# Kernel optimization log

Hardware: AMD Instinct MI355X
Metric: run time of the kernel (lower is better)

The kernel has to match this reference:

```python
import jax, jax.numpy as jnp
import numpy as np

NUM_EXPERTS = 8
TOP_K = 2
HIDDEN = 1024
INTER = 2048
BATCH, SEQ = 2, 2048


def setup_inputs() -> dict:
    key = jax.random.key(0)
    k1, k2, k3, k4 = jax.random.split(key, 4)
    hidden_states = jax.random.normal(k1, (BATCH, SEQ, HIDDEN), dtype=jnp.float32)
    # 0.02 init scale keeps router softmax unsaturated and activations sane
    router_w = jax.random.normal(k2, (NUM_EXPERTS, HIDDEN), dtype=jnp.float32) * 0.02
    up_w = jax.random.normal(k3, (NUM_EXPERTS, HIDDEN, INTER), dtype=jnp.float32) * 0.02
    down_w = jax.random.normal(k4, (NUM_EXPERTS, INTER, HIDDEN), dtype=jnp.float32) * 0.02
    return {"hidden_states": hidden_states, "router_w": router_w, "up_w": up_w, "down_w": down_w}


def reference(hidden_states, router_w, up_w, down_w):
    batch, seq_len, hidden = hidden_states.shape
    flat = hidden_states.reshape(-1, hidden)            # [N, H]
    num_tokens = flat.shape[0]

    router_logits = flat @ router_w.T                   # [N, E]
    router_probs = jax.nn.softmax(router_logits, axis=-1)
    top_weights, top_indices = jax.lax.top_k(router_probs, TOP_K)  # [N, k]
    top_weights = top_weights / jnp.sum(top_weights, axis=-1, keepdims=True)

    # scatter normalized top-k weights into a dense [N, E] mask
    rows = jnp.arange(num_tokens)[:, None]
    expert_mask = jnp.zeros((num_tokens, NUM_EXPERTS), dtype=flat.dtype)
    expert_mask = expert_mask.at[rows, top_indices].set(top_weights)

    # dense path: all experts on all tokens via batched matmul
    h = jnp.einsum('nh,ehf->enf', flat, up_w)           # [E, N, F]
    h = jax.nn.gelu(h, approximate=False)               # torch nn.GELU default = erf
    expert_out = jnp.einsum('enf,efh->enh', h, down_w)  # [E, N, H]
    output = jnp.einsum('enh,ne->nh', expert_out, expert_mask)
    output = output.reshape(batch, seq_len, hidden)

    # load-balancing aux loss; f is computed under no_grad in torch
    one_hot = jnp.zeros((num_tokens, NUM_EXPERTS), dtype=jnp.float32)
    one_hot = one_hot.at[rows, top_indices].set(1.0)
    f = jax.lax.stop_gradient(jnp.sum(one_hot, axis=0) / (num_tokens * TOP_K))
    P = jnp.mean(router_probs, axis=0)
    aux_loss = NUM_EXPERTS * jnp.sum(f * P)
    return output, aux_loss
```

## Files before the change

### kernel.cpp

```cpp
#include <hip/hip_runtime.h>
#include <math.h>

#define NE 8
#define HD 1024
#define FD 2048
#define NT 4096
#define NSLOT (NT * 2)

typedef __attribute__((ext_vector_type(8))) _Float16 half8;
typedef __attribute__((ext_vector_type(4))) float floatx4;

__device__ __forceinline__ void gload_lds(const _Float16* g, _Float16* l) {
  __builtin_amdgcn_global_load_lds(
      (const __attribute__((address_space(1))) unsigned int*)g,
      (__attribute__((address_space(3))) unsigned int*)l, 16, 0, 0);
}

__global__ __launch_bounds__(256) void transpose_cvt(const float* __restrict__ in,
                                                     _Float16* __restrict__ outp,
                                                     int R, int C) {
  __shared__ float t[32][132];
  int e = blockIdx.z;
  int r0 = blockIdx.x * 32, c0 = blockIdx.y * 128;
  int tid = threadIdx.x;
  int f4c = tid & 31, rr = tid >> 5;
  const float* src = in + (size_t)e * R * C;
#pragma unroll
  for (int i = 0; i < 4; i++) {
    float4 v = *(const float4*)(src + (size_t)(r0 + rr + 8 * i) * C + c0 + f4c * 4);
    *(float4*)&t[rr + 8 * i][f4c * 4] = v;
  }
  __syncthreads();
  _Float16* dst = outp + (size_t)e * R * C;
  int oc = tid >> 1, rh = (tid & 1) * 16;
  union { _Float16 h[8]; uint4 v; } o;
#pragma unroll
  for (int k2 = 0; k2 < 2; k2++) {
#pragma unroll
    for (int k = 0; k < 8; k++) o.h[k] = (_Float16)t[rh + k2 * 8 + k][oc];
    *(uint4*)(dst + (size_t)(c0 + oc) * R + r0 + rh + k2 * 8) = o.v;
  }
}

__global__ __launch_bounds__(256) void router_probs_kernel(
    const float* __restrict__ x, const float* __restrict__ rw, _Float16* __restrict__ xh,
    float* __restrict__ probs, int* __restrict__ sel_e, float* __restrict__ sel_w) {
  int n = blockIdx.x * 4 + (threadIdx.x >> 6);
  int lane = threadIdx.x & 63;
  const float* xr = x + (size_t)n * HD;
  float xv[16];
#pragma unroll
  for (int t = 0; t < 16; t++) xv[t] = xr[lane + 64 * t];
  _Float16* xhr = xh + (size_t)n * HD;
#pragma unroll
  for (int t = 0; t < 16; t++) xhr[lane + 64 * t] = (_Float16)xv[t];
  float logits[NE];
#pragma unroll
  for (int e = 0; e < NE; e++) {
    const float* w = rw + (size_t)e * HD;
    float acc = 0.f;
#pragma unroll
    for (int t = 0; t < 16; t++) acc += xv[t] * w[lane + 64 * t];
    for (int off = 32; off > 0; off >>= 1) acc += __shfl_down(acc, off);
    logits[e] = acc;
  }
  if (lane == 0) {
    float mx = logits[0];
#pragma unroll
    for (int e = 1; e < NE; e++) mx = fmaxf(mx, logits[e]);
    float p[NE]; float s = 0.f;
#pragma unroll
    for (int e = 0; e < NE; e++) { p[e] = expf(logits[e] - mx); s += p[e]; }
    float inv = 1.f / s;
#pragma unroll
    for (int e = 0; e < NE; e++) { p[e] *= inv; probs[n * NE + e] = p[e]; }
    int i1 = 0;
#pragma unroll
    for (int e = 1; e < NE; e++) if (p[e] > p[i1]) i1 = e;
    int i2 = -1; float p2 = -1.f;
#pragma unroll
    for (int e = 0; e < NE; e++) {
      if (e == i1) continue;
      if (p[e] > p2) { p2 = p[e]; i2 = e; }
    }
    float wn = 1.f / (p[i1] + p[i2]);
    sel_e[n * 2 + 0] = i1; sel_w[n * 2 + 0] = p[i1] * wn;
    sel_e[n * 2 + 1] = i2; sel_w[n * 2 + 1] = p[i2] * wn;
  }
}

__global__ __launch_bounds__(1024) void router_reduce_kernel(
    const float* __restrict__ probs, const int* __restrict__ sel_e,
    int* __restrict__ counts, int* __restrict__ offs, int* __restrict__ cursor,
    float* __restrict__ aux_out) {
  int t = threadIdx.x;
  int lane = t & 63, wave = t >> 6;
  float ps[NE];
  int cn[NE];
#pragma unroll
  for (int e = 0; e < NE; e++) { ps[e] = 0.f; cn[e] = 0; }
  for (int r = t; r < NT; r += 1024) {
    const float* pr = probs + (size_t)r * NE;
#pragma unroll
    for (int e = 0; e < NE; e++) ps[e] += pr[e];
  }
  for (int i = t; i < NSLOT; i += 1024) {
    int e = sel_e[i];
#pragma unroll
    for (int j = 0; j < NE; j++) cn[j] += (e == j) ? 1 : 0;
  }
  for (int off = 32; off > 0; off >>= 1) {
#pragma unroll
    for (int e = 0; e < NE; e++) {
      ps[e] += __shfl_down(ps[e], off);
      cn[e] += __shfl_down(cn[e], off);
    }
  }
  __shared__ float sps[16][NE];
  __shared__ int scn[16][NE];
  if (lane == 0) {
#pragma unroll
    for (int e = 0; e < NE; e++) { sps[wave][e] = ps[e]; scn[wave][e] = cn[e]; }
  }
  __syncthreads();
  if (t == 0) {
    float tot_p[NE]; int tot_c[NE];
#pragma unroll
    for (int e = 0; e < NE; e++) { tot_p[e] = 0.f; tot_c[e] = 0; }
    for (int w = 0; w < 16; w++)
#pragma unroll
      for (int e = 0; e < NE; e++) { tot_p[e] += sps[w][e]; tot_c[e] += scn[w][e]; }
    int o = 0;
    float aux = 0.f;
    for (int e = 0; e < NE; e++) {
      counts[e] = tot_c[e];
      offs[e] = o; o += tot_c[e];
      cursor[e] = 0;
      aux += ((float)tot_c[e] / (float)NSLOT) * (tot_p[e] / (float)NT);
    }
    aux_out[0] = (float)NE * aux;
  }
}

__global__ __launch_bounds__(256) void build_gather(
    const int* __restrict__ sel_e, const float* __restrict__ sel_w,
    const int* __restrict__ offs, int* __restrict__ cursor,
    int* __restrict__ gtok, float* __restrict__ gw, int* __restrict__ srow) {
  __shared__ int lh[NE], lbase[NE];
  int t = threadIdx.x;
  int i = blockIdx.x * 256 + t;
  if (t < NE) lh[t] = 0;
  __syncthreads();
  int e = sel_e[i];
  int lrank = atomicAdd(&lh[e], 1);
  __syncthreads();
  if (t < NE) lbase[t] = atomicAdd(&cursor[t], lh[t]);
  __syncthreads();
  int row = offs[e] + lbase[e] + lrank;
  gtok[row] = i >> 1;
  gw[row] = sel_w[i];
  srow[i] = row;
}

template <int KDIM, int NDIM, bool IS_UP>
__global__ __launch_bounds__(256, 3) void moe_gemm2(
    const _Float16* __restrict__ Abase, const _Float16* __restrict__ Bt,
    const int* __restrict__ counts, const int* __restrict__ offs,
    const int* __restrict__ gtok, const float* __restrict__ gw,
    _Float16* __restrict__ Hout, float* __restrict__ Dout) {
  int e = blockIdx.x;
  int cnt = counts[e];
  int m0 = blockIdx.y * 128;
  if (m0 >= cnt) return;
  int n0 = blockIdx.z * 128;
  int off = offs[e];

  __shared__ __align__(16) _Float16 As[128 * 64];
  __shared__ __align__(16) _Float16 Bs[128 * 64];

  int tid = threadIdx.x;
  int lane = tid & 63, wave = tid >> 6;
  int wm = (wave >> 1) * 64, wn = (wave & 1) * 64;

  int srow8 = lane >> 3;
  int chunk = (lane & 7) ^ srow8;
  const _Float16* ga[4];
  const _Float16* gb[4];
  _Float16* lA[4];
  _Float16* lB[4];
#pragma unroll
  for (int j = 0; j < 4; j++) {
    int r = wave * 32 + j * 8 + srow8;
    int am = m0 + r;
    if (am > cnt - 1) am = cnt - 1;
    if (IS_UP) {
      ga[j] = Abase + (size_t)gtok[off + am] * KDIM + chunk * 8;
    } else {
      ga[j] = Abase + (size_t)(off + am) * KDIM + chunk * 8;
    }
    gb[j] = Bt + ((size_t)e * NDIM + n0 + r) * KDIM + chunk * 8;
    lA[j] = As + (wave * 32 + j * 8) * 64;
    lB[j] = Bs + (wave * 32 + j * 8) * 64;
  }

  floatx4 acc[4][4];
#pragma unroll
  for (int i = 0; i < 4; i++)
#pragma unroll
    for (int j = 0; j < 4; j++) acc[i][j] = (floatx4){0.f, 0.f, 0.f, 0.f};

  int fr = lane & 15, g = lane >> 4;
  int sw0 = ((g) ^ (fr & 7)) * 8;
  int sw1 = ((4 + g) ^ (fr & 7)) * 8;

  for (int kt = 0; kt < KDIM / 64; kt++) {
    __syncthreads();
#pragma unroll
    for (int j = 0; j < 4; j++) gload_lds(ga[j], lA[j]);
#pragma unroll
    for (int j = 0; j < 4; j++) gload_lds(gb[j], lB[j]);
#pragma unroll
    for (int j = 0; j < 4; j++) { ga[j] += 64; gb[j] += 64; }
    __syncthreads();

    half8 af[4], bfv[4];
#pragma unroll
    for (int t = 0; t < 4; t++) {
      af[t] = *(const half8*)(As + (wm + t * 16 + fr) * 64 + sw0);
      bfv[t] = *(const half8*)(Bs + (wn + t * 16 + fr) * 64 + sw0);
    }
#pragma unroll
    for (int i = 0; i < 4; i++)
#pragma unroll
      for (int j = 0; j < 4; j++)
        acc[i][j] = __builtin_amdgcn_mfma_f32_16x16x32_f16(af[i], bfv[j], acc[i][j], 0, 0, 0);
#pragma unroll
    for (int t = 0; t < 4; t++) {
      af[t] = *(const half8*)(As + (wm + t * 16 + fr) * 64 + sw1);
      bfv[t] = *(const half8*)(Bs + (wn + t * 16 + fr) * 64 + sw1);
    }
#pragma unroll
    for (int i = 0; i < 4; i++)
#pragma unroll
      for (int j = 0; j < 4; j++)
        acc[i][j] = __builtin_amdgcn_mfma_f32_16x16x32_f16(af[i], bfv[j], acc[i][j], 0, 0, 0);
  }

  int cq = (lane >> 4) * 4, cc = lane & 15;
#pragma unroll
  for (int i = 0; i < 4; i++) {
#pragma unroll
    for (int r = 0; r < 4; r++) {
      int m = wm + i * 16 + cq + r;
      if (m0 + m < cnt) {
        if (IS_UP) {
          float w = gw[off + m0 + m];
          _Float16* hrow = Hout + (size_t)(off + m0 + m) * NDIM + n0;
#pragma unroll
          for (int j = 0; j < 4; j++) {
            float v = acc[i][j][r];
            float gl = 0.5f * v * (1.f + erff(v * 0.70710678118f));
            hrow[wn + j * 16 + cc] = (_Float16)(gl * w);
          }
        } else {
          float* orow = Dout + (size_t)(off + m0 + m) * NDIM + n0;
#pragma unroll
          for (int j = 0; j < 4; j++) orow[wn + j * 16 + cc] = acc[i][j][r];
        }
      }
    }
  }
}

__global__ __launch_bounds__(256) void combine_kernel(
    const float* __restrict__ Dout, const int* __restrict__ srow,
    float* __restrict__ out) {
  int n = blockIdx.x;
  int t = threadIdx.x;
  int r0 = srow[n * 2], r1 = srow[n * 2 + 1];
  float4 a = *(const float4*)(Dout + (size_t)r0 * HD + t * 4);
  float4 b = *(const float4*)(Dout + (size_t)r1 * HD + t * 4);
  float4 c; c.x = a.x + b.x; c.y = a.y + b.y; c.z = a.z + b.z; c.w = a.w + b.w;
  *(float4*)(out + (size_t)n * HD + t * 4) = c;
}

extern "C" void kernel_launch(void* const* d_in, const int* in_sizes, int n_in,
                              void* d_out, int out_size, void* d_ws, size_t ws_size,
                              hipStream_t stream) {
  const float* x = (const float*)d_in[0];
  const float* rw = (const float*)d_in[1];
  const float* up_w = (const float*)d_in[2];
  const float* dn_w = (const float*)d_in[3];
  float* out = (float*)d_out;

  char* ws = (char*)d_ws;
  _Float16* Xh   = (_Float16*)(ws + 0);
  _Float16* Wut  = (_Float16*)(ws + 8388608);
  float*    Dout = (float*)(ws + 0);
  _Float16* Wdt  = (_Float16*)(ws + 41943040);
  _Float16* Hbuf = (_Float16*)(ws + 75497472);
  char* tail = ws + 109051904;
  int*   gtok   = (int*)(tail + 0);
  float* gw     = (float*)(tail + 32768);
  int*   sel_e  = (int*)(tail + 65536);
  float* sel_w  = (float*)(tail + 98304);
  int*   srow   = (int*)(tail + 131072);
  float* probs  = (float*)(tail + 163840);
  int*   counts = (int*)(tail + 294912);
  int*   offs   = (int*)(tail + 294944);
  int*   cursor = (int*)(tail + 294976);

  transpose_cvt<<<dim3(HD / 32, FD / 128, NE), 256, 0, stream>>>(up_w, Wut, HD, FD);
  transpose_cvt<<<dim3(FD / 32, HD / 128, NE), 256, 0, stream>>>(dn_w, Wdt, FD, HD);
  router_probs_kernel<<<NT / 4, 256, 0, stream>>>(x, rw, Xh, probs, sel_e, sel_w);
  router_reduce_kernel<<<1, 1024, 0, stream>>>(probs, sel_e, counts, offs, cursor,
                                               out + (size_t)NT * HD);
  build_gather<<<NSLOT / 256, 256, 0, stream>>>(sel_e, sel_w, offs, cursor, gtok, gw, srow);

  moe_gemm2<HD, FD, true><<<dim3(NE, 32, FD / 128), 256, 0, stream>>>(
      Xh, Wut, counts, offs, gtok, gw, Hbuf, nullptr);
  moe_gemm2<FD, HD, false><<<dim3(NE, 32, HD / 128), 256, 0, stream>>>(
      Hbuf, Wdt, counts, offs, gtok, gw, nullptr, Dout);
  combine_kernel<<<NT, 256, 0, stream>>>(Dout, srow, out);
}
```

Baseline: 322.8 us.

## Load MFMA operands directly from global memory, dropping LDS staging

```diff
diff --git a/kernel.cpp b/kernel.cpp
--- a/kernel.cpp
+++ b/kernel.cpp
@@ -9,12 +9,6 @@
 
 typedef __attribute__((ext_vector_type(8))) _Float16 half8;
 typedef __attribute__((ext_vector_type(4))) float floatx4;
-
-__device__ __forceinline__ void gload_lds(const _Float16* g, _Float16* l) {
-  __builtin_amdgcn_global_load_lds(
-      (const __attribute__((address_space(1))) unsigned int*)g,
-      (__attribute__((address_space(3))) unsigned int*)l, 16, 0, 0);
-}
 
 __global__ __launch_bounds__(256) void transpose_cvt(const float* __restrict__ in,
                                                      _Float16* __restrict__ outp,
@@ -163,7 +157,7 @@
 }
 
 template <int KDIM, int NDIM, bool IS_UP>
-__global__ __launch_bounds__(256, 3) void moe_gemm2(
+__global__ __launch_bounds__(256, 4) void moe_gemm_d(
     const _Float16* __restrict__ Abase, const _Float16* __restrict__ Bt,
     const int* __restrict__ counts, const int* __restrict__ offs,
     const int* __restrict__ gtok, const float* __restrict__ gw,
@@ -175,32 +169,22 @@
   int n0 = blockIdx.z * 128;
   int off = offs[e];
 
-  __shared__ __align__(16) _Float16 As[128 * 64];
-  __shared__ __align__(16) _Float16 Bs[128 * 64];
-
-  int tid = threadIdx.x;
-  int lane = tid & 63, wave = tid >> 6;
+  int lane = threadIdx.x & 63, wave = threadIdx.x >> 6;
   int wm = (wave >> 1) * 64, wn = (wave & 1) * 64;
-
-  int srow8 = lane >> 3;
-  int chunk = (lane & 7) ^ srow8;
-  const _Float16* ga[4];
-  const _Float16* gb[4];
-  _Float16* lA[4];
-  _Float16* lB[4];
-#pragma unroll
-  for (int j = 0; j < 4; j++) {
-    int r = wave * 32 + j * 8 + srow8;
-    int am = m0 + r;
+  int fr = lane & 15, g = lane >> 4;
+
+  const _Float16* ap[4];
+  const _Float16* bp[4];
+#pragma unroll
+  for (int t = 0; t < 4; t++) {
+    int am = m0 + wm + t * 16 + fr;
     if (am > cnt - 1) am = cnt - 1;
     if (IS_UP) {
-      ga[j] = Abase + (size_t)gtok[off + am] * KDIM + chunk * 8;
+      ap[t] = Abase + (size_t)gtok[off + am] * KDIM + g * 8;
     } else {
-      ga[j] = Abase + (size_t)(off + am) * KDIM + chunk * 8;
-    }
-    gb[j] = Bt + ((size_t)e * NDIM + n0 + r) * KDIM + chunk * 8;
-    lA[j] = As + (wave * 32 + j * 8) * 64;
-    lB[j] = Bs + (wave * 32 + j * 8) * 64;
+      ap[t] = Abase + (size_t)(off + am) * KDIM + g * 8;
+    }
+    bp[t] = Bt + ((size_t)e * NDIM + n0 + wn + t * 16 + fr) * KDIM + g * 8;
   }
 
   floatx4 acc[4][4];
@@ -209,25 +193,12 @@
 #pragma unroll
     for (int j = 0; j < 4; j++) acc[i][j] = (floatx4){0.f, 0.f, 0.f, 0.f};
 
-  int fr = lane & 15, g = lane >> 4;
-  int sw0 = ((g) ^ (fr & 7)) * 8;
-  int sw1 = ((4 + g) ^ (fr & 7)) * 8;
-
   for (int kt = 0; kt < KDIM / 64; kt++) {
-    __syncthreads();
-#pragma unroll
-    for (int j = 0; j < 4; j++) gload_lds(ga[j], lA[j]);
-#pragma unroll
-    for (int j = 0; j < 4; j++) gload_lds(gb[j], lB[j]);
-#pragma unroll
-    for (int j = 0; j < 4; j++) { ga[j] += 64; gb[j] += 64; }
-    __syncthreads();
-
     half8 af[4], bfv[4];
 #pragma unroll
     for (int t = 0; t < 4; t++) {
-      af[t] = *(const half8*)(As + (wm + t * 16 + fr) * 64 + sw0);
-      bfv[t] = *(const half8*)(Bs + (wn + t * 16 + fr) * 64 + sw0);
+      af[t] = *(const half8*)(ap[t]);
+      bfv[t] = *(const half8*)(bp[t]);
     }
 #pragma unroll
     for (int i = 0; i < 4; i++)
@@ -236,14 +207,16 @@
         acc[i][j] = __builtin_amdgcn_mfma_f32_16x16x32_f16(af[i], bfv[j], acc[i][j], 0, 0, 0);
 #pragma unroll
     for (int t = 0; t < 4; t++) {
-      af[t] = *(const half8*)(As + (wm + t * 16 + fr) * 64 + sw1);
-      bfv[t] = *(const half8*)(Bs + (wn + t * 16 + fr) * 64 + sw1);
+      af[t] = *(const half8*)(ap[t] + 32);
+      bfv[t] = *(const half8*)(bp[t] + 32);
     }
 #pragma unroll
     for (int i = 0; i < 4; i++)
 #pragma unroll
       for (int j = 0; j < 4; j++)
         acc[i][j] = __builtin_amdgcn_mfma_f32_16x16x32_f16(af[i], bfv[j], acc[i][j], 0, 0, 0);
+#pragma unroll
+    for (int t = 0; t < 4; t++) { ap[t] += 64; bp[t] += 64; }
   }
 
   int cq = (lane >> 4) * 4, cc = lane & 15;
@@ -317,9 +290,9 @@
                                                out + (size_t)NT * HD);
   build_gather<<<NSLOT / 256, 256, 0, stream>>>(sel_e, sel_w, offs, cursor, gtok, gw, srow);
 
-  moe_gemm2<HD, FD, true><<<dim3(NE, 32, FD / 128), 256, 0, stream>>>(
+  moe_gemm_d<HD, FD, true><<<dim3(NE, 32, FD / 128), 256, 0, stream>>>(
       Xh, Wut, counts, offs, gtok, gw, Hbuf, nullptr);
-  moe_gemm2<FD, HD, false><<<dim3(NE, 32, HD / 128), 256, 0, stream>>>(
+  moe_gemm_d<FD, HD, false><<<dim3(NE, 32, HD / 128), 256, 0, stream>>>(
       Hbuf, Wdt, counts, offs, gtok, gw, nullptr, Dout);
   combine_kernel<<<NT, 256, 0, stream>>>(Dout, srow, out);
 }
```

Result: slower. 661.4 us (+104.9%).
